# Kernel optimization log

Measured on AMD Instinct MI355X. Metric: run time of the kernel, lower is better.

## Reference

```python
import jax, jax.numpy as jnp
import numpy as np

D = 128      # internal_dimensions
L = 4        # num_edge_convs
N = 100000   # nodes
E = 800000   # edges
G = 64       # graphs
IN = 4       # in_channels


def _ln(x, g, b):
    m = jnp.mean(x, -1, keepdims=True)
    v = jnp.mean((x - m) ** 2, -1, keepdims=True)
    return (x - m) * jax.lax.rsqrt(v + 1e-5) * g + b


def _gelu(x):
    return jax.nn.gelu(x, approximate=False)  # torch nn.GELU default (erf)


def _seg_mean(x, seg, n):
    s = jax.ops.segment_sum(x, seg, num_segments=n)
    c = jax.ops.segment_sum(jnp.ones((x.shape[0], 1), x.dtype), seg, num_segments=n)
    return s / jnp.maximum(c, 1.0)


def _seg_max(x, seg, n):
    m = jax.ops.segment_max(x, seg, num_segments=n)
    return jnp.where(jnp.isfinite(m), m, 0.0)  # empty segments -> 0 (PyG convention)


def _forward(x, edge_index, batch, num_graphs,
             in_W1, in_b1, in_g1, in_bn1, in_W2, in_b2, in_g2, in_bn2,
             pre_g, pre_b, cW1, cb1, cg1, cbb1, cW2, cb2, cg2, cbb2, pW, pb,
             ag_g, ag_b,
             kW1, kb1, kg1, kbb1, kW2, kb2, kg2, kbb2,
             kW3, kb3, kg3, kbb3, kW4, kb4):
    n = x.shape[0]
    # input_net: Linear -> LN -> GELU -> Linear -> LN   (dropout=0, eval)
    h = _gelu(_ln(x @ in_W1 + in_b1, in_g1, in_bn1))
    h = _ln(h @ in_W2 + in_b2, in_g2, in_bn2)

    x_in_max = _seg_max(h, batch, num_graphs)
    x_in_mean = _seg_mean(h, batch, num_graphs)

    src, dst = edge_index[0], edge_index[1]  # PyG: message from src (x_j) to dst (x_i)
    xcur = h
    for l in range(L):
        identity = xcur
        hn = _ln(xcur, pre_g[l], pre_b[l])
        xi = hn[dst]            # [E, D]
        xj = hn[src]            # [E, D]
        m = jnp.concatenate([xi, xj - xi], axis=-1)       # [E, 2D]
        m = _gelu(_ln(m @ cW1[l] + cb1[l], cg1[l], cbb1[l]))
        m = _gelu(_ln(m @ cW2[l] + cb2[l], cg2[l], cbb2[l]))
        a_max = _seg_max(m, dst, n)
        a_mean = _seg_mean(m, dst, n)
        aggr = jnp.concatenate([a_max, a_mean], axis=-1)  # [N, 2D]
        xcur = identity + aggr @ pW[l] + pb[l]

    xcur = _ln(xcur, ag_g, ag_b)
    x_g_max = _seg_max(xcur, batch, num_graphs)
    x_g_mean = _seg_mean(xcur, batch, num_graphs)

    xp = jnp.concatenate([x_in_max, x_in_mean, x_g_max, x_g_mean], axis=-1)  # [G, 4D]
    z = _gelu(_ln(xp @ kW1 + kb1, kg1, kbb1))
    z = _gelu(_ln(z @ kW2 + kb2, kg2, kbb2))
    z = _gelu(_ln(z @ kW3 + kb3, kg3, kbb3))
    return z @ kW4 + kb4  # [G, 1]


def setup_inputs() -> dict:
    key = jax.random.key(0)
    ks = iter(jax.random.split(key, 64))
    def W(shape, fan):
        return jax.random.normal(next(ks), shape, jnp.float32) * np.float32((2.0 / fan) ** 0.5)
    inp = {}
    inp["x"] = jax.random.normal(next(ks), (N, IN), jnp.float32)
    inp["edge_index"] = jax.random.randint(next(ks), (2, E), 0, N)
    inp["batch"] = jnp.sort(jax.random.randint(next(ks), (N,), 0, G))
    inp["num_graphs"] = G
    inp["in_W1"] = W((IN, D), IN); inp["in_b1"] = jnp.zeros((D,), jnp.float32)
    inp["in_g1"] = jnp.ones((D,), jnp.float32); inp["in_bn1"] = jnp.zeros((D,), jnp.float32)
    inp["in_W2"] = W((D, D), D); inp["in_b2"] = jnp.zeros((D,), jnp.float32)
    inp["in_g2"] = jnp.ones((D,), jnp.float32); inp["in_bn2"] = jnp.zeros((D,), jnp.float32)
    inp["pre_g"] = jnp.ones((L, D), jnp.float32); inp["pre_b"] = jnp.zeros((L, D), jnp.float32)
    inp["cW1"] = W((L, 2 * D, D), 2 * D); inp["cb1"] = jnp.zeros((L, D), jnp.float32)
    inp["cg1"] = jnp.ones((L, D), jnp.float32); inp["cbb1"] = jnp.zeros((L, D), jnp.float32)
    inp["cW2"] = W((L, D, D), D); inp["cb2"] = jnp.zeros((L, D), jnp.float32)
    inp["cg2"] = jnp.ones((L, D), jnp.float32); inp["cbb2"] = jnp.zeros((L, D), jnp.float32)
    inp["pW"] = W((L, 2 * D, D), 2 * D); inp["pb"] = jnp.zeros((L, D), jnp.float32)
    inp["ag_g"] = jnp.ones((D,), jnp.float32); inp["ag_b"] = jnp.zeros((D,), jnp.float32)
    inp["kW1"] = W((4 * D, D), 4 * D); inp["kb1"] = jnp.zeros((D,), jnp.float32)
    inp["kg1"] = jnp.ones((D,), jnp.float32); inp["kbb1"] = jnp.zeros((D,), jnp.float32)
    inp["kW2"] = W((D, D), D); inp["kb2"] = jnp.zeros((D,), jnp.float32)
    inp["kg2"] = jnp.ones((D,), jnp.float32); inp["kbb2"] = jnp.zeros((D,), jnp.float32)
    inp["kW3"] = W((D, D // 4), D); inp["kb3"] = jnp.zeros((D // 4,), jnp.float32)
    inp["kg3"] = jnp.ones((D // 4,), jnp.float32); inp["kbb3"] = jnp.zeros((D // 4,), jnp.float32)
    inp["kW4"] = W((D // 4, 1), D // 4); inp["kb4"] = jnp.zeros((1,), jnp.float32)
    return inp


def reference(x, edge_index, batch, num_graphs,
              in_W1, in_b1, in_g1, in_bn1, in_W2, in_b2, in_g2, in_bn2,
              pre_g, pre_b, cW1, cb1, cg1, cbb1, cW2, cb2, cg2, cbb2, pW, pb,
              ag_g, ag_b,
              kW1, kb1, kg1, kbb1, kW2, kb2, kg2, kbb2,
              kW3, kb3, kg3, kbb3, kW4, kb4):
    return _forward(x, edge_index, batch, num_graphs,
                    in_W1, in_b1, in_g1, in_bn1, in_W2, in_b2, in_g2, in_bn2,
                    pre_g, pre_b, cW1, cb1, cg1, cbb1, cW2, cb2, cg2, cbb2, pW, pb,
                    ag_g, ag_b,
                    kW1, kb1, kg1, kbb1, kW2, kb2, kg2, kbb2,
                    kW3, kb3, kg3, kbb3, kW4, kb4)
```

## Files before the change

kernel.cpp:

```cpp
#include <hip/hip_runtime.h>
#include <hip/hip_bf16.h>
#include <math.h>

__device__ __forceinline__ float geluf(float x) {
    return 0.5f * x * (1.0f + erff(x * 0.70710678118654752f));
}
__device__ __forceinline__ unsigned fmap(float f) {
    unsigned u = __float_as_uint(f);
    return ((int)u < 0) ? ~u : (u | 0x80000000u);
}
__device__ __forceinline__ float funmap(unsigned m) {
    return __uint_as_float((m & 0x80000000u) ? (m ^ 0x80000000u) : ~m);
}
#define MAPNEGINF 0x007FFFFFu
__device__ __forceinline__ float wred64(float v) {
#pragma unroll
    for (int m = 1; m < 64; m <<= 1) v += __shfl_xor(v, m);
    return v;
}

__device__ __forceinline__ void stage_wq(float* Ws, const float* __restrict__ src, int t) {
#pragma unroll
    for (int it = 0; it < 4; ++it) {
        const int idx = it * 1024 + (t << 2);
        *(float4*)(Ws + idx) = *(const float4*)(src + idx);
    }
}

__device__ __forceinline__ void kloop_q(const float* As, const float* Ws, float (&acc)[4][8],
                                        const int r0, const int ogc, const int kb) {
#pragma unroll
    for (int kk = 0; kk < 32; kk += 4) {
        const float4 a0 = *(const float4*)(As + (r0 + 0) * 132 + kb + kk);
        const float4 a1 = *(const float4*)(As + (r0 + 1) * 132 + kb + kk);
        const float4 a2 = *(const float4*)(As + (r0 + 2) * 132 + kb + kk);
        const float4 a3 = *(const float4*)(As + (r0 + 3) * 132 + kb + kk);
#define MAD8(R, AV)                                                                     \
    {                                                                                   \
        acc[R][0] += (AV)*wA.x; acc[R][1] += (AV)*wA.y; acc[R][2] += (AV)*wA.z;         \
        acc[R][3] += (AV)*wA.w; acc[R][4] += (AV)*wB.x; acc[R][5] += (AV)*wB.y;         \
        acc[R][6] += (AV)*wB.z; acc[R][7] += (AV)*wB.w;                                 \
    }
#define KSTEP(J, C)                                                                     \
    {                                                                                   \
        const float4 wA = *(const float4*)(Ws + (kk + (J)) * 128 + ogc);                \
        const float4 wB = *(const float4*)(Ws + (kk + (J)) * 128 + 64 + ogc);           \
        MAD8(0, a0.C) MAD8(1, a1.C) MAD8(2, a2.C) MAD8(3, a3.C)                         \
    }
        KSTEP(0, x) KSTEP(1, y) KSTEP(2, z) KSTEP(3, w)
#undef KSTEP
#undef MAD8
    }
}

__global__ void k_zero(unsigned* __restrict__ p, int n) {
    const int i = blockIdx.x * 256 + threadIdx.x;
    if (i < n) p[i] = 0u;
}

__global__ void k_copyu(const unsigned* __restrict__ a, const unsigned* __restrict__ b,
                        unsigned* __restrict__ ac, unsigned* __restrict__ bc, int n) {
    const int i = blockIdx.x * 256 + threadIdx.x;
    if (i < n) {
        ac[i] = a[i];
        bc[i] = b[i];
    }
}

__global__ void k_count(const int* __restrict__ ei, unsigned* __restrict__ deg, int E) {
    const int e = blockIdx.x * 256 + threadIdx.x;
    if (e < E) atomicAdd(deg + ei[E + e], 1u);
}

__global__ void k_scan1(const unsigned* __restrict__ deg, unsigned* __restrict__ excl,
                        unsigned* __restrict__ bsum, int n) {
    __shared__ unsigned sh[256];
    const int t = threadIdx.x;
    const int base = blockIdx.x * 1024 + t * 4;
    unsigned v0 = (base + 0 < n) ? deg[base + 0] : 0u;
    unsigned v1 = (base + 1 < n) ? deg[base + 1] : 0u;
    unsigned v2 = (base + 2 < n) ? deg[base + 2] : 0u;
    unsigned v3 = (base + 3 < n) ? deg[base + 3] : 0u;
    const unsigned s = v0 + v1 + v2 + v3;
    sh[t] = s;
    __syncthreads();
    for (int off = 1; off < 256; off <<= 1) {
        unsigned x = 0;
        if (t >= off) x = sh[t - off];
        __syncthreads();
        if (t >= off) sh[t] += x;
        __syncthreads();
    }
    const unsigned ebase = sh[t] - s;
    if (base + 0 < n) excl[base + 0] = ebase;
    if (base + 1 < n) excl[base + 1] = ebase + v0;
    if (base + 2 < n) excl[base + 2] = ebase + v0 + v1;
    if (base + 3 < n) excl[base + 3] = ebase + v0 + v1 + v2;
    if (t == 255) bsum[blockIdx.x] = sh[255];
}

__global__ void k_scan2(unsigned* __restrict__ bsum, int nb) {
    __shared__ unsigned sh[256];
    const int t = threadIdx.x;
    const unsigned v = (t < nb) ? bsum[t] : 0u;
    sh[t] = v;
    __syncthreads();
    for (int off = 1; off < 256; off <<= 1) {
        unsigned x = 0;
        if (t >= off) x = sh[t - off];
        __syncthreads();
        if (t >= off) sh[t] += x;
        __syncthreads();
    }
    if (t < nb) bsum[t] = sh[t] - v;
}

__global__ void k_scan3(unsigned* __restrict__ excl, const unsigned* __restrict__ bsum, int n) {
    const int t = threadIdx.x;
    const int base = blockIdx.x * 1024 + t * 4;
    const unsigned add = bsum[blockIdx.x];
#pragma unroll
    for (int j = 0; j < 4; ++j)
        if (base + j < n) excl[base + j] += add;
}

__global__ void k_scatter(const int* __restrict__ ei, unsigned* __restrict__ cursor,
                          int* __restrict__ eperm, int E) {
    const int e = blockIdx.x * 256 + threadIdx.x;
    if (e < E) {
        const unsigned pos = atomicAdd(cursor + ei[E + e], 1u);
        eperm[pos] = e;
    }
}

__global__ void k_in1(const float* __restrict__ x, const float* __restrict__ W1,
                      const float* __restrict__ b1, const float* __restrict__ g1,
                      const float* __restrict__ bn1, float* __restrict__ h, int n) {
    const int t = threadIdx.x, lane = t & 63, wave = t >> 6;
    const int d0 = lane << 1;
    const float2 w0 = *(const float2*)(W1 + d0);
    const float2 w1 = *(const float2*)(W1 + 128 + d0);
    const float2 w2 = *(const float2*)(W1 + 256 + d0);
    const float2 w3 = *(const float2*)(W1 + 384 + d0);
    const float2 bb = *(const float2*)(b1 + d0);
    const float2 gg = *(const float2*)(g1 + d0);
    const float2 nn = *(const float2*)(bn1 + d0);
    const int stride = gridDim.x * 4;
    for (int node = blockIdx.x * 4 + wave; node < n; node += stride) {
        const float4 xv = *(const float4*)(x + (size_t)node * 4);
        float h0 = bb.x + xv.x * w0.x + xv.y * w1.x + xv.z * w2.x + xv.w * w3.x;
        float h1 = bb.y + xv.x * w0.y + xv.y * w1.y + xv.z * w2.y + xv.w * w3.y;
        const float s = wred64(h0 + h1), q = wred64(h0 * h0 + h1 * h1);
        const float mean = s * 0.0078125f, var = q * 0.0078125f - mean * mean;
        const float rs = rsqrtf(var + 1e-5f);
        h0 = geluf((h0 - mean) * rs * gg.x + nn.x);
        h1 = geluf((h1 - mean) * rs * gg.y + nn.y);
        *(float2*)(h + (size_t)node * 128 + d0) = make_float2(h0, h1);
    }
}

__global__ __launch_bounds__(256, 3) void k_in2(const float* __restrict__ A,
                                                const float* __restrict__ W,
                                                const float* __restrict__ bias,
                                                const float* __restrict__ g,
                                                const float* __restrict__ b,
                                                float* __restrict__ C, int n) {
    __shared__ float As[64 * 132];
    __shared__ float Ws[4096];
    const int t = threadIdx.x;
    const int n0 = blockIdx.x * 64;
    {
        const int r = t >> 2, c0 = (t & 3) << 5;
        const int row = n0 + r;
        const bool ok = row < n;
#pragma unroll
        for (int j = 0; j < 8; ++j) {
            const int col = c0 + (j << 2);
            float4 v = make_float4(0.f, 0.f, 0.f, 0.f);
            if (ok) v = *(const float4*)(A + (size_t)row * 128 + col);
            *(float4*)(As + r * 132 + col) = v;
        }
    }
    float acc[4][8];
#pragma unroll
    for (int r = 0; r < 4; ++r)
#pragma unroll
        for (int o = 0; o < 8; ++o) acc[r][o] = 0.f;
    const int og = t & 15, eg = t >> 4;
    const int ogc = og << 2, r0 = eg << 2;
#pragma unroll
    for (int q4 = 0; q4 < 4; ++q4) {
        stage_wq(Ws, W + q4 * 4096, t);
        __syncthreads();
        kloop_q(As, Ws, acc, r0, ogc, q4 * 32);
        __syncthreads();
    }
    const float4 bA = *(const float4*)(bias + ogc);
    const float4 bB = *(const float4*)(bias + 64 + ogc);
    const float4 gA = *(const float4*)(g + ogc);
    const float4 gB = *(const float4*)(g + 64 + ogc);
    const float4 lA = *(const float4*)(b + ogc);
    const float4 lB = *(const float4*)(b + 64 + ogc);
#pragma unroll
    for (int r = 0; r < 4; ++r) {
        float v[8];
        v[0] = acc[r][0] + bA.x; v[1] = acc[r][1] + bA.y;
        v[2] = acc[r][2] + bA.z; v[3] = acc[r][3] + bA.w;
        v[4] = acc[r][4] + bB.x; v[5] = acc[r][5] + bB.y;
        v[6] = acc[r][6] + bB.z; v[7] = acc[r][7] + bB.w;
        float s = 0.f, q = 0.f;
#pragma unroll
        for (int o = 0; o < 8; ++o) { s += v[o]; q += v[o] * v[o]; }
#pragma unroll
        for (int m = 1; m < 16; m <<= 1) { s += __shfl_xor(s, m); q += __shfl_xor(q, m); }
        const float mean = s * 0.0078125f;
        const float var = q * 0.0078125f - mean * mean;
        const float rs = rsqrtf(var + 1e-5f);
        const int row = n0 + r0 + r;
        if (row < n) {
            *(float4*)(C + (size_t)row * 128 + ogc) = make_float4(
                (v[0] - mean) * rs * gA.x + lA.x, (v[1] - mean) * rs * gA.y + lA.y,
                (v[2] - mean) * rs * gA.z + lA.z, (v[3] - mean) * rs * gA.w + lA.w);
            *(float4*)(C + (size_t)row * 128 + 64 + ogc) = make_float4(
                (v[4] - mean) * rs * gB.x + lB.x, (v[5] - mean) * rs * gB.y + lB.y,
                (v[6] - mean) * rs * gB.z + lB.z, (v[7] - mean) * rs * gB.w + lB.w);
        }
    }
}

__global__ void k_ln(const float* __restrict__ in, const float* __restrict__ g,
                     const float* __restrict__ b, float* __restrict__ out, int n) {
    const int t = threadIdx.x, lane = t & 63, wave = t >> 6;
    const int d0 = lane << 1;
    const float ga = g[d0], gb = g[d0 + 1], ba = b[d0], bb = b[d0 + 1];
    const int stride = gridDim.x * 4;
    for (int node = blockIdx.x * 4 + wave; node < n; node += stride) {
        const float2 v = *(const float2*)(in + (size_t)node * 128 + d0);
        const float s = wred64(v.x + v.y), q = wred64(v.x * v.x + v.y * v.y);
        const float mean = s * 0.0078125f, var = q * 0.0078125f - mean * mean;
        const float rs = rsqrtf(var + 1e-5f);
        *(float2*)(out + (size_t)node * 128 + d0) =
            make_float2((v.x - mean) * rs * ga + ba, (v.y - mean) * rs * gb + bb);
    }
}

__global__ void k_wxj(const float* __restrict__ c, float* __restrict__ Wx,
                      float* __restrict__ Wj) {
    const int idx = blockIdx.x * 256 + threadIdx.x;
    const float a = c[idx], b = c[16384 + idx];
    Wx[idx] = a - b;
    Wj[idx] = b;
}

__global__ __launch_bounds__(256, 3) void k_pq(const float* __restrict__ xcur,
                                               const float* __restrict__ g,
                                               const float* __restrict__ b,
                                               const float* __restrict__ Wx,
                                               const float* __restrict__ Wj,
                                               const float* __restrict__ cb1,
                                               float* __restrict__ P, float* __restrict__ Q,
                                               int n) {
    __shared__ float As[64 * 132];
    __shared__ float Ws[4096];
    __shared__ float sg[128], sb[128];
    const int t = threadIdx.x;
    const int n0 = blockIdx.x * 64;
    if (t < 128) { sg[t] = g[t]; sb[t] = b[t]; }
    __syncthreads();
    {
        const int r = t >> 2, c0 = (t & 3) << 5;
        const int row = n0 + r;
        const bool ok = row < n;
        float4 v4[8];
        float s = 0.f, q = 0.f;
        if (ok) {
#pragma unroll
            for (int j = 0; j < 8; ++j) {
                v4[j] = *(const float4*)(xcur + (size_t)row * 128 + c0 + (j << 2));
                s += v4[j].x + v4[j].y + v4[j].z + v4[j].w;
                q += v4[j].x * v4[j].x + v4[j].y * v4[j].y + v4[j].z * v4[j].z +
                     v4[j].w * v4[j].w;
            }
        } else {
#pragma unroll
            for (int j = 0; j < 8; ++j) v4[j] = make_float4(0.f, 0.f, 0.f, 0.f);
        }
        s += __shfl_xor(s, 1); s += __shfl_xor(s, 2);
        q += __shfl_xor(q, 1); q += __shfl_xor(q, 2);
        const float mean = s * 0.0078125f;
        const float var = q * 0.0078125f - mean * mean;
        const float rs = rsqrtf(var + 1e-5f);
#pragma unroll
        for (int j = 0; j < 8; ++j) {
            const int c = c0 + (j << 2);
            As[r * 132 + c + 0] = (v4[j].x - mean) * rs * sg[c + 0] + sb[c + 0];
            As[r * 132 + c + 1] = (v4[j].y - mean) * rs * sg[c + 1] + sb[c + 1];
            As[r * 132 + c + 2] = (v4[j].z - mean) * rs * sg[c + 2] + sb[c + 2];
            As[r * 132 + c + 3] = (v4[j].w - mean) * rs * sg[c + 3] + sb[c + 3];
        }
    }
    float accP[4][8], accQ[4][8];
#pragma unroll
    for (int r = 0; r < 4; ++r)
#pragma unroll
        for (int o = 0; o < 8; ++o) { accP[r][o] = 0.f; accQ[r][o] = 0.f; }
    const int og = t & 15, eg = t >> 4;
    const int ogc = og << 2, r0 = eg << 2;
#pragma unroll
    for (int q4 = 0; q4 < 4; ++q4) {
        stage_wq(Ws, Wx + q4 * 4096, t);
        __syncthreads();
        kloop_q(As, Ws, accP, r0, ogc, q4 * 32);
        __syncthreads();
    }
#pragma unroll
    for (int q4 = 0; q4 < 4; ++q4) {
        stage_wq(Ws, Wj + q4 * 4096, t);
        __syncthreads();
        kloop_q(As, Ws, accQ, r0, ogc, q4 * 32);
        __syncthreads();
    }
    const float4 bA = *(const float4*)(cb1 + ogc);
    const float4 bB = *(const float4*)(cb1 + 64 + ogc);
#pragma unroll
    for (int r = 0; r < 4; ++r) {
        const int row = n0 + r0 + r;
        if (row < n) {
            *(float4*)(P + (size_t)row * 128 + ogc) =
                make_float4(accP[r][0] + bA.x, accP[r][1] + bA.y, accP[r][2] + bA.z,
                            accP[r][3] + bA.w);
            *(float4*)(P + (size_t)row * 128 + 64 + ogc) =
                make_float4(accP[r][4] + bB.x, accP[r][5] + bB.y, accP[r][6] + bB.z,
                            accP[r][7] + bB.w);
            *(float4*)(Q + (size_t)row * 128 + ogc) =
                make_float4(accQ[r][0], accQ[r][1], accQ[r][2], accQ[r][3]);
            *(float4*)(Q + (size_t)row * 128 + 64 + ogc) =
                make_float4(accQ[r][4], accQ[r][5], accQ[r][6], accQ[r][7]);
        }
    }
}

__global__ __launch_bounds__(256, 3) void k_edge(
    const float* __restrict__ P, const float* __restrict__ Q, const int* __restrict__ ei,
    const int* __restrict__ eperm, const float* __restrict__ W2, const float* __restrict__ g1,
    const float* __restrict__ b1, const float* __restrict__ cb2, const float* __restrict__ g2,
    const float* __restrict__ b2, const unsigned* __restrict__ rowend,
    const unsigned* __restrict__ degc, float* __restrict__ amax, float* __restrict__ asum,
    float* __restrict__ recmax, float* __restrict__ recsum, int* __restrict__ recid, int E) {
    __shared__ float Us[64 * 132];
    __shared__ float Ws[4096];
    __shared__ int sdst[64], ssrc[64], sdg[64];
    __shared__ float scb2[128], sg2[128], sb2[128];
    const int t = threadIdx.x;
    const int base = blockIdx.x * 512;
    if (t >= 128) {
        const int d = t - 128;
        scb2[d] = cb2[d];
        sg2[d] = g2[d];
        sb2[d] = b2[d];
    }
    const int lane = t & 63, wave = t >> 6;
    const int d0 = lane << 1;
    const float g1a = g1[d0], g1b = g1[d0 + 1], b1a = b1[d0], b1b = b1[d0 + 1];
    const int og = t & 15, eg = t >> 4;
    const int ogc = og << 2, r0 = eg << 2;
    int cur = -1, istart = 0;
    float vmax = -INFINITY, vsum = 0.f;
    int id0 = -1, id1 = -1;

    for (int s8 = 0; s8 < 8; ++s8) {
        const int sb = base + s8 * 64;
        __syncthreads();
        if (t < 64) {
            const int idx = sb + t;
            const int e = eperm[idx < E ? idx : (E - 1)];
            ssrc[t] = ei[e];
            const int d = ei[E + e];
            sdg[t] = d;
            sdst[t] = (idx < E) ? d : -1;
        }
        __syncthreads();
#pragma unroll
        for (int half = 0; half < 2; ++half) {
            float2 pv[8], qv[8];
#pragma unroll
            for (int u = 0; u < 8; ++u) {
                const int i = ((half * 8 + u) << 2) + wave;
                pv[u] = *(const float2*)(P + (size_t)sdg[i] * 128 + d0);
                qv[u] = *(const float2*)(Q + (size_t)ssrc[i] * 128 + d0);
            }
#pragma unroll
            for (int u = 0; u < 8; ++u) {
                const int i = ((half * 8 + u) << 2) + wave;
                const float x0 = pv[u].x + qv[u].x, x1 = pv[u].y + qv[u].y;
                const float s = wred64(x0 + x1);
                const float q = wred64(x0 * x0 + x1 * x1);
                const float mean = s * 0.0078125f;
                const float var = q * 0.0078125f - mean * mean;
                const float rs = rsqrtf(var + 1e-5f);
                const float y0 = geluf((x0 - mean) * rs * g1a + b1a);
                const float y1 = geluf((x1 - mean) * rs * g1b + b1b);
                *(float2*)(Us + i * 132 + d0) = make_float2(y0, y1);
            }
        }
        float acc[4][8];
#pragma unroll
        for (int r = 0; r < 4; ++r)
#pragma unroll
            for (int o = 0; o < 8; ++o) acc[r][o] = 0.f;
#pragma unroll
        for (int q4 = 0; q4 < 4; ++q4) {
            stage_wq(Ws, W2 + q4 * 4096, t);
            __syncthreads();
            kloop_q(Us, Ws, acc, r0, ogc, q4 * 32);
            __syncthreads();
        }
#pragma unroll
        for (int r = 0; r < 4; ++r) {
            float v[8];
            float s = 0.f, q = 0.f;
#pragma unroll
            for (int o = 0; o < 8; ++o) {
                const int col = (o < 4) ? (ogc + o) : (64 + ogc + o - 4);
                v[o] = acc[r][o] + scb2[col];
                s += v[o];
                q += v[o] * v[o];
            }
#pragma unroll
            for (int m = 1; m < 16; m <<= 1) { s += __shfl_xor(s, m); q += __shfl_xor(q, m); }
            const float mean = s * 0.0078125f;
            const float var = q * 0.0078125f - mean * mean;
            const float rs = rsqrtf(var + 1e-5f);
#pragma unroll
            for (int o = 0; o < 8; ++o) {
                const int col = (o < 4) ? (ogc + o) : (64 + ogc + o - 4);
                v[o] = geluf((v[o] - mean) * rs * sg2[col] + sb2[col]);
            }
            *(float4*)(Us + (r0 + r) * 132 + ogc) = make_float4(v[0], v[1], v[2], v[3]);
            *(float4*)(Us + (r0 + r) * 132 + 64 + ogc) = make_float4(v[4], v[5], v[6], v[7]);
        }
        __syncthreads();
        if (t < 128) {
            for (int i = 0; i < 64; ++i) {
                const int dn = sdst[i];
                const int gi = s8 * 64 + i;
                if (dn != cur) {
                    if (cur >= 0) {
                        const unsigned re = rowend[cur];
                        const unsigned rs0 = re - degc[cur];
                        const unsigned ps = (unsigned)(base + istart);
                        const unsigned pe = (unsigned)(base + gi);
                        if (ps == rs0 && pe == re) {
                            amax[(size_t)cur * 128 + t] = vmax;
                            asum[(size_t)cur * 128 + t] = vsum;
                        } else {
                            const int slot = (istart == 0) ? 0 : 1;
                            const size_t ro = (size_t)(2 * blockIdx.x + slot) * 128 + t;
                            recmax[ro] = vmax;
                            recsum[ro] = vsum;
                            if (slot == 0) id0 = cur; else id1 = cur;
                        }
                    }
                    cur = dn;
                    istart = gi;
                    vmax = -INFINITY;
                    vsum = 0.f;
                }
                if (dn >= 0) {
                    const float v = Us[i * 132 + t];
                    vmax = fmaxf(vmax, v);
                    vsum += v;
                }
            }
        }
    }
    if (t < 128 && cur >= 0) {
        const int iend = min(512, E - base);
        const unsigned re = rowend[cur];
        const unsigned rs0 = re - degc[cur];
        const unsigned ps = (unsigned)(base + istart);
        const unsigned pe = (unsigned)(base + iend);
        if (ps == rs0 && pe == re) {
            amax[(size_t)cur * 128 + t] = vmax;
            asum[(size_t)cur * 128 + t] = vsum;
        } else {
            const int slot = (istart == 0) ? 0 : 1;
            const size_t ro = (size_t)(2 * blockIdx.x + slot) * 128 + t;
            recmax[ro] = vmax;
            recsum[ro] = vsum;
            if (slot == 0) id0 = cur; else id1 = cur;
        }
    }
    if (t == 0) {
        recid[2 * blockIdx.x] = id0;
        recid[2 * blockIdx.x + 1] = id1;
    }
}

__global__ void k_merge(const unsigned* __restrict__ rowend, const unsigned* __restrict__ degc,
                        const float* __restrict__ recmax, const float* __restrict__ recsum,
                        const int* __restrict__ recid, float* __restrict__ amax,
                        float* __restrict__ asum, int n) {
    const int node = blockIdx.x * 2 + (threadIdx.x >> 7);
    const int t = threadIdx.x & 127;
    if (node >= n) return;
    const unsigned dg = degc[node];
    if (dg == 0u) {
        amax[(size_t)node * 128 + t] = 0.f;
        asum[(size_t)node * 128 + t] = 0.f;
        return;
    }
    const unsigned re = rowend[node], rs = re - dg;
    const int b0 = rs >> 9, b1 = (re - 1) >> 9;
    if (b0 == b1) return;
    float m = -INFINITY, s = 0.f;
    for (int b = b0; b <= b1; ++b) {
#pragma unroll
        for (int sl = 0; sl < 2; ++sl) {
            if (recid[2 * b + sl] == node) {
                const size_t ro = (size_t)(2 * b + sl) * 128 + t;
                m = fmaxf(m, recmax[ro]);
                s += recsum[ro];
            }
        }
    }
    amax[(size_t)node * 128 + t] = m;
    asum[(size_t)node * 128 + t] = s;
}

__global__ __launch_bounds__(256, 3) void k_update(const float* __restrict__ amax,
                                                   const float* __restrict__ asum,
                                                   const unsigned* __restrict__ degc,
                                                   const float* __restrict__ pW,
                                                   const float* __restrict__ pb,
                                                   float* __restrict__ xcur, int n) {
    __shared__ float As[64 * 132];
    __shared__ float Ws[4096];
    const int t = threadIdx.x;
    const int n0 = blockIdx.x * 64;
    const int og = t & 15, eg = t >> 4;
    const int ogc = og << 2, r0 = eg << 2;
    float acc[4][8];
#pragma unroll
    for (int r = 0; r < 4; ++r)
#pragma unroll
        for (int o = 0; o < 8; ++o) acc[r][o] = 0.f;
    const int r = t >> 2, c0 = (t & 3) << 5;
    const int row = n0 + r;
    const bool ok = row < n;
#pragma unroll
    for (int pass = 0; pass < 2; ++pass) {
        if (pass == 0) {
#pragma unroll
            for (int j = 0; j < 8; ++j) {
                const int col = c0 + (j << 2);
                float4 v = make_float4(0.f, 0.f, 0.f, 0.f);
                if (ok) v = *(const float4*)(amax + (size_t)row * 128 + col);
                *(float4*)(As + r * 132 + col) = v;
            }
        } else {
            float inv = 0.f;
            if (ok) {
                const unsigned dv = degc[row];
                inv = 1.f / (float)(dv < 1u ? 1u : dv);
            }
#pragma unroll
            for (int j = 0; j < 8; ++j) {
                const int col = c0 + (j << 2);
                float4 v = make_float4(0.f, 0.f, 0.f, 0.f);
                if (ok) {
                    const float4 sv = *(const float4*)(asum + (size_t)row * 128 + col);
                    v = make_float4(sv.x * inv, sv.y * inv, sv.z * inv, sv.w * inv);
                }
                *(float4*)(As + r * 132 + col) = v;
            }
        }
#pragma unroll
        for (int q4 = 0; q4 < 4; ++q4) {
            stage_wq(Ws, pW + (size_t)(pass * 128 + q4 * 32) * 128, t);
            __syncthreads();
            kloop_q(As, Ws, acc, r0, ogc, q4 * 32);
            __syncthreads();
        }
    }
    const float4 bA = *(const float4*)(pb + ogc);
    const float4 bB = *(const float4*)(pb + 64 + ogc);
#pragma unroll
    for (int rr = 0; rr < 4; ++rr) {
        const int orow = n0 + r0 + rr;
        if (orow < n) {
            const float4 x0 = *(const float4*)(xcur + (size_t)orow * 128 + ogc);
            const float4 x1 = *(const float4*)(xcur + (size_t)orow * 128 + 64 + ogc);
            *(float4*)(xcur + (size_t)orow * 128 + ogc) =
                make_float4(x0.x + acc[rr][0] + bA.x, x0.y + acc[rr][1] + bA.y,
                            x0.z + acc[rr][2] + bA.z, x0.w + acc[rr][3] + bA.w);
            *(float4*)(xcur + (size_t)orow * 128 + 64 + ogc) =
                make_float4(x1.x + acc[rr][4] + bB.x, x1.y + acc[rr][5] + bB.y,
                            x1.z + acc[rr][6] + bB.z, x1.w + acc[rr][7] + bB.w);
        }
    }
}

__global__ void k_pool_init(unsigned* __restrict__ gmax1, float* __restrict__ gsum1,
                            unsigned* __restrict__ gcount1, unsigned* __restrict__ gmax2,
                            float* __restrict__ gsum2, unsigned* __restrict__ gcount2, int ng) {
    const int i = blockIdx.x * 256 + threadIdx.x;
    if (i < ng * 128) {
        gmax1[i] = MAPNEGINF;
        gsum1[i] = 0.f;
        gmax2[i] = MAPNEGINF;
        gsum2[i] = 0.f;
    }
    if (i < ng) {
        gcount1[i] = 0u;
        gcount2[i] = 0u;
    }
}

__global__ void k_pool(const float* __restrict__ in, const int* __restrict__ batch,
                       unsigned* __restrict__ gmax, float* __restrict__ gsum,
                       unsigned* __restrict__ gcount, int n) {
    const int t = threadIdx.x;
    if (t >= 128) return;
    const int per = (n + gridDim.x - 1) / gridDim.x;
    const int i0 = blockIdx.x * per;
    const int i1 = min(n, i0 + per);
    if (i0 >= i1) return;
    int cur = batch[i0];
    float vmax = -INFINITY, vsum = 0.f;
    unsigned cnt = 0;
    for (int i = i0; i < i1; ++i) {
        const int g = batch[i];
        if (g != cur) {
            atomicMax(gmax + (size_t)cur * 128 + t, fmap(vmax));
            atomicAdd(gsum + (size_t)cur * 128 + t, vsum);
            if (t == 0) atomicAdd(gcount + cur, cnt);
            cur = g;
            vmax = -INFINITY;
            vsum = 0.f;
            cnt = 0;
        }
        const float v = in[(size_t)i * 128 + t];
        vmax = fmaxf(vmax, v);
        vsum += v;
        cnt++;
    }
    atomicMax(gmax + (size_t)cur * 128 + t, fmap(vmax));
    atomicAdd(gsum + (size_t)cur * 128 + t, vsum);
    if (t == 0) atomicAdd(gcount + cur, cnt);
}

__global__ void k_xp(const unsigned* __restrict__ gmax1, const float* __restrict__ gsum1,
                     const unsigned* __restrict__ gcount1, const unsigned* __restrict__ gmax2,
                     const float* __restrict__ gsum2, const unsigned* __restrict__ gcount2,
                     float* __restrict__ xp) {
    const int g = blockIdx.x, d = threadIdx.x;
    const unsigned c1u = gcount1[g], c2u = gcount2[g];
    const float c1 = (float)(c1u < 1u ? 1u : c1u);
    const float c2 = (float)(c2u < 1u ? 1u : c2u);
    const unsigned m1 = gmax1[g * 128 + d], m2 = gmax2[g * 128 + d];
    xp[g * 512 + d] = (m1 == MAPNEGINF) ? 0.f : funmap(m1);
    xp[g * 512 + 128 + d] = gsum1[g * 128 + d] / c1;
    xp[g * 512 + 256 + d] = (m2 == MAPNEGINF) ? 0.f : funmap(m2);
    xp[g * 512 + 384 + d] = gsum2[g * 128 + d] / c2;
}

__global__ __launch_bounds__(64) void k_know(
    const float* __restrict__ xp, const float* __restrict__ kW1, const float* __restrict__ kb1,
    const float* __restrict__ kg1, const float* __restrict__ kbb1, const float* __restrict__ kW2,
    const float* __restrict__ kb2, const float* __restrict__ kg2, const float* __restrict__ kbb2,
    const float* __restrict__ kW3, const float* __restrict__ kb3, const float* __restrict__ kg3,
    const float* __restrict__ kbb3, const float* __restrict__ kW4, const float* __restrict__ kb4,
    float* __restrict__ out) {
    __shared__ float sh[512];
    __shared__ float s3[32];
    const int l = threadIdx.x, g = blockIdx.x;
    const int d0 = l << 1;
    *(float4*)(sh + l * 8) = *(const float4*)(xp + g * 512 + l * 8);
    *(float4*)(sh + l * 8 + 4) = *(const float4*)(xp + g * 512 + l * 8 + 4);
    __syncthreads();
    float a0 = kb1[d0], a1 = kb1[d0 + 1];
    for (int k = 0; k < 512; ++k) {
        const float u = sh[k];
        const float2 w = *(const float2*)(kW1 + k * 128 + d0);
        a0 += u * w.x;
        a1 += u * w.y;
    }
    {
        const float s = wred64(a0 + a1), q = wred64(a0 * a0 + a1 * a1);
        const float mean = s * 0.0078125f, var = q * 0.0078125f - mean * mean;
        const float rs = rsqrtf(var + 1e-5f);
        a0 = geluf((a0 - mean) * rs * kg1[d0] + kbb1[d0]);
        a1 = geluf((a1 - mean) * rs * kg1[d0 + 1] + kbb1[d0 + 1]);
    }
    __syncthreads();
    sh[d0] = a0;
    sh[d0 + 1] = a1;
    __syncthreads();
    float b0v = kb2[d0], b1v = kb2[d0 + 1];
    for (int k = 0; k < 128; ++k) {
        const float u = sh[k];
        const float2 w = *(const float2*)(kW2 + k * 128 + d0);
        b0v += u * w.x;
        b1v += u * w.y;
    }
    {
        const float s = wred64(b0v + b1v), q = wred64(b0v * b0v + b1v * b1v);
        const float mean = s * 0.0078125f, var = q * 0.0078125f - mean * mean;
        const float rs = rsqrtf(var + 1e-5f);
        b0v = geluf((b0v - mean) * rs * kg2[d0] + kbb2[d0]);
        b1v = geluf((b1v - mean) * rs * kg2[d0 + 1] + kbb2[d0 + 1]);
    }
    __syncthreads();
    sh[d0] = b0v;
    sh[d0 + 1] = b1v;
    __syncthreads();
    const int d3 = (l & 15) << 1;
    float c0 = kb3[d3], c1 = kb3[d3 + 1];
    for (int k = 0; k < 128; ++k) {
        const float u = sh[k];
        const float2 w = *(const float2*)(kW3 + k * 32 + d3);
        c0 += u * w.x;
        c1 += u * w.y;
    }
    {
        float s = c0 + c1, q = c0 * c0 + c1 * c1;
#pragma unroll
        for (int m = 1; m < 16; m <<= 1) {
            s += __shfl_xor(s, m);
            q += __shfl_xor(q, m);
        }
        const float mean = s * 0.03125f, var = q * 0.03125f - mean * mean;
        const float rs = rsqrtf(var + 1e-5f);
        c0 = geluf((c0 - mean) * rs * kg3[d3] + kbb3[d3]);
        c1 = geluf((c1 - mean) * rs * kg3[d3 + 1] + kbb3[d3 + 1]);
    }
    if (l < 16) {
        s3[d3] = c0;
        s3[d3 + 1] = c1;
    }
    __syncthreads();
    if (l == 0) {
        float rr = kb4[0];
        for (int k = 0; k < 32; ++k) rr += s3[k] * kW4[k];
        out[g] = rr;
    }
}

extern "C" void kernel_launch(void* const* d_in, const int* in_sizes, int n_in, void* d_out,
                              int out_size, void* d_ws, size_t ws_size, hipStream_t stream) {
    const int N = in_sizes[0] / 4;
    const int E = in_sizes[1] / 2;
    const int G = 64;
    const int L = 4;

    const float* x = (const float*)d_in[0];
    const int* ei = (const int*)d_in[1];
    const int* batch = (const int*)d_in[2];
    const float* inW1 = (const float*)d_in[4];
    const float* inb1 = (const float*)d_in[5];
    const float* ing1 = (const float*)d_in[6];
    const float* inbn1 = (const float*)d_in[7];
    const float* inW2 = (const float*)d_in[8];
    const float* inb2 = (const float*)d_in[9];
    const float* ing2 = (const float*)d_in[10];
    const float* inbn2 = (const float*)d_in[11];
    const float* pre_g = (const float*)d_in[12];
    const float* pre_b = (const float*)d_in[13];
    const float* cW1 = (const float*)d_in[14];
    const float* cb1 = (const float*)d_in[15];
    const float* cg1 = (const float*)d_in[16];
    const float* cbb1 = (const float*)d_in[17];
    const float* cW2 = (const float*)d_in[18];
    const float* cb2 = (const float*)d_in[19];
    const float* cg2 = (const float*)d_in[20];
    const float* cbb2 = (const float*)d_in[21];
    const float* pW = (const float*)d_in[22];
    const float* pb = (const float*)d_in[23];
    const float* ag_g = (const float*)d_in[24];
    const float* ag_b = (const float*)d_in[25];
    const float* kW1 = (const float*)d_in[26];
    const float* kb1 = (const float*)d_in[27];
    const float* kg1 = (const float*)d_in[28];
    const float* kbb1 = (const float*)d_in[29];
    const float* kW2 = (const float*)d_in[30];
    const float* kb2 = (const float*)d_in[31];
    const float* kg2 = (const float*)d_in[32];
    const float* kbb2 = (const float*)d_in[33];
    const float* kW3 = (const float*)d_in[34];
    const float* kb3 = (const float*)d_in[35];
    const float* kg3 = (const float*)d_in[36];
    const float* kbb3 = (const float*)d_in[37];
    const float* kW4 = (const float*)d_in[38];
    const float* kb4 = (const float*)d_in[39];
    float* out = (float*)d_out;

    const int nblkE = (E + 511) / 512;

    char* wsb = (char*)d_ws;
    size_t off = 0;
    auto ALC = [&](size_t bytes) {
        void* p = wsb + off;
        off = (off + bytes + 255) & ~(size_t)255;
        return p;
    };
    const size_t NB = (size_t)N * 128 * 4;
    float* xcur = (float*)ALC(NB);
    float* Pb = (float*)ALC(NB);
    float* Qb = (float*)ALC(NB);
    float* amax = (float*)ALC(NB);
    float* asum = (float*)ALC(NB);
    unsigned* deg = (unsigned*)ALC((size_t)N * 4);
    unsigned* cursor = (unsigned*)ALC((size_t)N * 4);
    unsigned* degc = (unsigned*)ALC((size_t)N * 4);
    unsigned* rowend = (unsigned*)ALC((size_t)N * 4);
    unsigned* bsum = (unsigned*)ALC(4096);
    int* eperm = (int*)ALC((size_t)E * 4);
    float* recmax = (float*)ALC((size_t)nblkE * 2 * 128 * 4);
    float* recsum = (float*)ALC((size_t)nblkE * 2 * 128 * 4);
    int* recid = (int*)ALC((size_t)nblkE * 2 * 4);
    float* Wx = (float*)ALC(65536);
    float* Wj = (float*)ALC(65536);
    unsigned* gmax1 = (unsigned*)ALC((size_t)G * 128 * 4);
    float* gsum1 = (float*)ALC((size_t)G * 128 * 4);
    unsigned* gcount1 = (unsigned*)ALC((size_t)G * 4);
    unsigned* gmax2 = (unsigned*)ALC((size_t)G * 128 * 4);
    float* gsum2 = (float*)ALC((size_t)G * 128 * 4);
    unsigned* gcount2 = (unsigned*)ALC((size_t)G * 4);
    float* xp = (float*)ALC((size_t)G * 512 * 4);

    if (off > ws_size) {
        k_zero<<<(out_size + 255) / 256, 256, 0, stream>>>((unsigned*)d_out, out_size);
        return;
    }

    k_zero<<<(N + 255) / 256, 256, 0, stream>>>(deg, N);
    k_count<<<(E + 255) / 256, 256, 0, stream>>>(ei, deg, E);
    const int nb = (N + 1023) / 1024;
    k_scan1<<<nb, 256, 0, stream>>>(deg, cursor, bsum, N);
    k_scan2<<<1, 256, 0, stream>>>(bsum, nb);
    k_scan3<<<nb, 256, 0, stream>>>(cursor, bsum, N);
    k_scatter<<<(E + 255) / 256, 256, 0, stream>>>(ei, cursor, eperm, E);
    k_copyu<<<(N + 255) / 256, 256, 0, stream>>>(deg, cursor, degc, rowend, N);

    const int gemmGrid = (N + 63) / 64;
    k_in1<<<1024, 256, 0, stream>>>(x, inW1, inb1, ing1, inbn1, Pb, N);
    k_in2<<<gemmGrid, 256, 0, stream>>>(Pb, inW2, inb2, ing2, inbn2, xcur, N);
    k_pool_init<<<(G * 128 + 255) / 256, 256, 0, stream>>>(gmax1, gsum1, gcount1, gmax2, gsum2,
                                                           gcount2, G);
    k_pool<<<512, 256, 0, stream>>>(xcur, batch, gmax1, gsum1, gcount1, N);

    for (int l = 0; l < L; ++l) {
        k_wxj<<<64, 256, 0, stream>>>(cW1 + (size_t)l * 32768, Wx, Wj);
        k_pq<<<gemmGrid, 256, 0, stream>>>(xcur, pre_g + l * 128, pre_b + l * 128, Wx, Wj,
                                           cb1 + l * 128, Pb, Qb, N);
        k_edge<<<nblkE, 256, 0, stream>>>(Pb, Qb, ei, eperm, cW2 + (size_t)l * 16384,
                                          cg1 + l * 128, cbb1 + l * 128, cb2 + l * 128,
                                          cg2 + l * 128, cbb2 + l * 128, rowend, degc, amax, asum,
                                          recmax, recsum, recid, E);
        k_merge<<<(N + 1) / 2, 256, 0, stream>>>(rowend, degc, recmax, recsum, recid, amax, asum,
                                                 N);
        k_update<<<gemmGrid, 256, 0, stream>>>(amax, asum, degc, pW + (size_t)l * 32768,
                                               pb + l * 128, xcur, N);
    }

    k_ln<<<1024, 256, 0, stream>>>(xcur, ag_g, ag_b, Pb, N);
    k_pool<<<512, 256, 0, stream>>>(Pb, batch, gmax2, gsum2, gcount2, N);
    k_xp<<<G, 128, 0, stream>>>(gmax1, gsum1, gcount1, gmax2, gsum2, gcount2, xp);
    k_know<<<G, 64, 0, stream>>>(xp, kW1, kb1, kg1, kbb1, kW2, kb2, kg2, kbb2, kW3, kb3, kg3,
                                 kbb3, kW4, kb4, out);
}
```

Measured before the change: 102.0 ms.

## Store per-node P/Q projections in bf16 and pre-sort edge src/dst arrays

The per-node P and Q projections that feed the edge kernel are now written as bf16, which halves the bytes of the random gathers over 800k edges per layer. The CSR scatter now writes sorted src and dst arrays directly, so the edge kernel no longer does an indirect lookup through eperm. The fused LN+dual-GEMM kernel is split into a separate LN pass plus two single-output GEMMs, and launch bounds drop from 3 to 2 blocks per CU. The risks are lost precision in the bf16 intermediates and the extra kernel launches and memory traffic for the normalized activations.

```diff
diff --git a/kernel.cpp b/kernel.cpp
--- a/kernel.cpp
+++ b/kernel.cpp
@@ -5,18 +5,23 @@
 __device__ __forceinline__ float geluf(float x) {
     return 0.5f * x * (1.0f + erff(x * 0.70710678118654752f));
 }
+#define MAPNEGINF 0x007FFFFFu
+__device__ __forceinline__ float funmap(unsigned m) {
+    return __uint_as_float((m & 0x80000000u) ? (m ^ 0x80000000u) : ~m);
+}
 __device__ __forceinline__ unsigned fmap(float f) {
     unsigned u = __float_as_uint(f);
     return ((int)u < 0) ? ~u : (u | 0x80000000u);
 }
-__device__ __forceinline__ float funmap(unsigned m) {
-    return __uint_as_float((m & 0x80000000u) ? (m ^ 0x80000000u) : ~m);
-}
-#define MAPNEGINF 0x007FFFFFu
 __device__ __forceinline__ float wred64(float v) {
 #pragma unroll
     for (int m = 1; m < 64; m <<= 1) v += __shfl_xor(v, m);
     return v;
+}
+__device__ __forceinline__ unsigned short bf16r(float f) {
+    unsigned u = __float_as_uint(f);
+    u += 0x7fffu + ((u >> 16) & 1u);
+    return (unsigned short)(u >> 16);
 }
 
 __device__ __forceinline__ void stage_wq(float* Ws, const float* __restrict__ src, int t) {
@@ -125,11 +130,14 @@
 }
 
 __global__ void k_scatter(const int* __restrict__ ei, unsigned* __restrict__ cursor,
-                          int* __restrict__ eperm, int E) {
+                          int* __restrict__ esrc, int* __restrict__ edst, int E) {
     const int e = blockIdx.x * 256 + threadIdx.x;
     if (e < E) {
-        const unsigned pos = atomicAdd(cursor + ei[E + e], 1u);
-        eperm[pos] = e;
+        const int s = ei[e];
+        const int d = ei[E + e];
+        const unsigned pos = atomicAdd(cursor + d, 1u);
+        esrc[pos] = s;
+        edst[pos] = d;
     }
 }
 
@@ -159,7 +167,7 @@
     }
 }
 
-__global__ __launch_bounds__(256, 3) void k_in2(const float* __restrict__ A,
+__global__ __launch_bounds__(256, 2) void k_in2(const float* __restrict__ A,
                                                 const float* __restrict__ W,
                                                 const float* __restrict__ bias,
                                                 const float* __restrict__ g,
@@ -252,101 +260,68 @@
     Wj[idx] = b;
 }
 
-__global__ __launch_bounds__(256, 3) void k_pq(const float* __restrict__ xcur,
-                                               const float* __restrict__ g,
-                                               const float* __restrict__ b,
-                                               const float* __restrict__ Wx,
-                                               const float* __restrict__ Wj,
-                                               const float* __restrict__ cb1,
-                                               float* __restrict__ P, float* __restrict__ Q,
-                                               int n) {
+__global__ __launch_bounds__(256, 2) void k_gemmh(const float* __restrict__ A,
+                                                  const float* __restrict__ W,
+                                                  const float* __restrict__ bias,
+                                                  unsigned short* __restrict__ C, int n) {
     __shared__ float As[64 * 132];
     __shared__ float Ws[4096];
-    __shared__ float sg[128], sb[128];
     const int t = threadIdx.x;
     const int n0 = blockIdx.x * 64;
-    if (t < 128) { sg[t] = g[t]; sb[t] = b[t]; }
-    __syncthreads();
     {
         const int r = t >> 2, c0 = (t & 3) << 5;
         const int row = n0 + r;
         const bool ok = row < n;
-        float4 v4[8];
-        float s = 0.f, q = 0.f;
-        if (ok) {
-#pragma unroll
-            for (int j = 0; j < 8; ++j) {
-                v4[j] = *(const float4*)(xcur + (size_t)row * 128 + c0 + (j << 2));
-                s += v4[j].x + v4[j].y + v4[j].z + v4[j].w;
-                q += v4[j].x * v4[j].x + v4[j].y * v4[j].y + v4[j].z * v4[j].z +
-                     v4[j].w * v4[j].w;
-            }
-        } else {
-#pragma unroll
-            for (int j = 0; j < 8; ++j) v4[j] = make_float4(0.f, 0.f, 0.f, 0.f);
-        }
-        s += __shfl_xor(s, 1); s += __shfl_xor(s, 2);
-        q += __shfl_xor(q, 1); q += __shfl_xor(q, 2);
-        const float mean = s * 0.0078125f;
-        const float var = q * 0.0078125f - mean * mean;
-        const float rs = rsqrtf(var + 1e-5f);
 #pragma unroll
         for (int j = 0; j < 8; ++j) {
-            const int c = c0 + (j << 2);
-            As[r * 132 + c + 0] = (v4[j].x - mean) * rs * sg[c + 0] + sb[c + 0];
-            As[r * 132 + c + 1] = (v4[j].y - mean) * rs * sg[c + 1] + sb[c + 1];
-            As[r * 132 + c + 2] = (v4[j].z - mean) * rs * sg[c + 2] + sb[c + 2];
-            As[r * 132 + c + 3] = (v4[j].w - mean) * rs * sg[c + 3] + sb[c + 3];
-        }
-    }
-    float accP[4][8], accQ[4][8];
+            const int col = c0 + (j << 2);
+            float4 v = make_float4(0.f, 0.f, 0.f, 0.f);
+            if (ok) v = *(const float4*)(A + (size_t)row * 128 + col);
+            *(float4*)(As + r * 132 + col) = v;
+        }
+    }
+    float acc[4][8];
 #pragma unroll
     for (int r = 0; r < 4; ++r)
 #pragma unroll
-        for (int o = 0; o < 8; ++o) { accP[r][o] = 0.f; accQ[r][o] = 0.f; }
+        for (int o = 0; o < 8; ++o) acc[r][o] = 0.f;
     const int og = t & 15, eg = t >> 4;
     const int ogc = og << 2, r0 = eg << 2;
 #pragma unroll
     for (int q4 = 0; q4 < 4; ++q4) {
-        stage_wq(Ws, Wx + q4 * 4096, t);
-        __syncthreads();
-        kloop_q(As, Ws, accP, r0, ogc, q4 * 32);
-        __syncthreads();
-    }
-#pragma unroll
-    for (int q4 = 0; q4 < 4; ++q4) {
-        stage_wq(Ws, Wj + q4 * 4096, t);
-        __syncthreads();
-        kloop_q(As, Ws, accQ, r0, ogc, q4 * 32);
-        __syncthreads();
-    }
-    const float4 bA = *(const float4*)(cb1 + ogc);
-    const float4 bB = *(const float4*)(cb1 + 64 + ogc);
+        stage_wq(Ws, W + q4 * 4096, t);
+        __syncthreads();
+        kloop_q(As, Ws, acc, r0, ogc, q4 * 32);
+        __syncthreads();
+    }
+    float4 bA = make_float4(0.f, 0.f, 0.f, 0.f), bB = bA;
+    if (bias) {
+        bA = *(const float4*)(bias + ogc);
+        bB = *(const float4*)(bias + 64 + ogc);
+    }
 #pragma unroll
     for (int r = 0; r < 4; ++r) {
         const int row = n0 + r0 + r;
         if (row < n) {
-            *(float4*)(P + (size_t)row * 128 + ogc) =
-                make_float4(accP[r][0] + bA.x, accP[r][1] + bA.y, accP[r][2] + bA.z,
-                            accP[r][3] + bA.w);
-            *(float4*)(P + (size_t)row * 128 + 64 + ogc) =
-                make_float4(accP[r][4] + bB.x, accP[r][5] + bB.y, accP[r][6] + bB.z,
-                            accP[r][7] + bB.w);
-            *(float4*)(Q + (size_t)row * 128 + ogc) =
-                make_float4(accQ[r][0], accQ[r][1], accQ[r][2], accQ[r][3]);
-            *(float4*)(Q + (size_t)row * 128 + 64 + ogc) =
-                make_float4(accQ[r][4], accQ[r][5], accQ[r][6], accQ[r][7]);
-        }
-    }
-}
-
-__global__ __launch_bounds__(256, 3) void k_edge(
-    const float* __restrict__ P, const float* __restrict__ Q, const int* __restrict__ ei,
-    const int* __restrict__ eperm, const float* __restrict__ W2, const float* __restrict__ g1,
-    const float* __restrict__ b1, const float* __restrict__ cb2, const float* __restrict__ g2,
-    const float* __restrict__ b2, const unsigned* __restrict__ rowend,
-    const unsigned* __restrict__ degc, float* __restrict__ amax, float* __restrict__ asum,
-    float* __restrict__ recmax, float* __restrict__ recsum, int* __restrict__ recid, int E) {
+            ushort4 u0, u1;
+            u0.x = bf16r(acc[r][0] + bA.x); u0.y = bf16r(acc[r][1] + bA.y);
+            u0.z = bf16r(acc[r][2] + bA.z); u0.w = bf16r(acc[r][3] + bA.w);
+            u1.x = bf16r(acc[r][4] + bB.x); u1.y = bf16r(acc[r][5] + bB.y);
+            u1.z = bf16r(acc[r][6] + bB.z); u1.w = bf16r(acc[r][7] + bB.w);
+            *(ushort4*)(C + (size_t)row * 128 + ogc) = u0;
+            *(ushort4*)(C + (size_t)row * 128 + 64 + ogc) = u1;
+        }
+    }
+}
+
+__global__ __launch_bounds__(256, 2) void k_edge(
+    const unsigned short* __restrict__ P, const unsigned short* __restrict__ Q,
+    const int* __restrict__ esrc, const int* __restrict__ edst, const float* __restrict__ W2,
+    const float* __restrict__ g1, const float* __restrict__ b1, const float* __restrict__ cb2,
+    const float* __restrict__ g2, const float* __restrict__ b2,
+    const unsigned* __restrict__ rowend, const unsigned* __restrict__ degc,
+    float* __restrict__ amax, float* __restrict__ asum, float* __restrict__ recmax,
+    float* __restrict__ recsum, int* __restrict__ recid, int E) {
     __shared__ float Us[64 * 132];
     __shared__ float Ws[4096];
     __shared__ int sdst[64], ssrc[64], sdg[64];
@@ -373,35 +348,29 @@
         __syncthreads();
         if (t < 64) {
             const int idx = sb + t;
-            const int e = eperm[idx < E ? idx : (E - 1)];
-            ssrc[t] = ei[e];
-            const int d = ei[E + e];
+            const int ci = idx < E ? idx : (E - 1);
+            ssrc[t] = esrc[ci];
+            const int d = edst[ci];
             sdg[t] = d;
             sdst[t] = (idx < E) ? d : -1;
         }
         __syncthreads();
-#pragma unroll
-        for (int half = 0; half < 2; ++half) {
-            float2 pv[8], qv[8];
-#pragma unroll
-            for (int u = 0; u < 8; ++u) {
-                const int i = ((half * 8 + u) << 2) + wave;
-                pv[u] = *(const float2*)(P + (size_t)sdg[i] * 128 + d0);
-                qv[u] = *(const float2*)(Q + (size_t)ssrc[i] * 128 + d0);
-            }
-#pragma unroll
-            for (int u = 0; u < 8; ++u) {
-                const int i = ((half * 8 + u) << 2) + wave;
-                const float x0 = pv[u].x + qv[u].x, x1 = pv[u].y + qv[u].y;
-                const float s = wred64(x0 + x1);
-                const float q = wred64(x0 * x0 + x1 * x1);
-                const float mean = s * 0.0078125f;
-                const float var = q * 0.0078125f - mean * mean;
-                const float rs = rsqrtf(var + 1e-5f);
-                const float y0 = geluf((x0 - mean) * rs * g1a + b1a);
-                const float y1 = geluf((x1 - mean) * rs * g1b + b1b);
-                *(float2*)(Us + i * 132 + d0) = make_float2(y0, y1);
-            }
+#pragma unroll 4
+        for (int p = 0; p < 16; ++p) {
+            const int i = (p << 2) + wave;
+            const unsigned pu = *(const unsigned*)(P + ((size_t)sdg[i] << 7) + d0);
+            const unsigned qu = *(const unsigned*)(Q + ((size_t)ssrc[i] << 7) + d0);
+            const float x0 = __uint_as_float(pu << 16) + __uint_as_float(qu << 16);
+            const float x1 =
+                __uint_as_float(pu & 0xffff0000u) + __uint_as_float(qu & 0xffff0000u);
+            const float s = wred64(x0 + x1);
+            const float q = wred64(x0 * x0 + x1 * x1);
+            const float mean = s * 0.0078125f;
+            const float var = q * 0.0078125f - mean * mean;
+            const float rs = rsqrtf(var + 1e-5f);
+            const float y0 = geluf((x0 - mean) * rs * g1a + b1a);
+            const float y1 = geluf((x1 - mean) * rs * g1b + b1b);
+            *(float2*)(Us + i * 132 + d0) = make_float2(y0, y1);
         }
         float acc[4][8];
 #pragma unroll
@@ -528,7 +497,7 @@
     asum[(size_t)node * 128 + t] = s;
 }
 
-__global__ __launch_bounds__(256, 3) void k_update(const float* __restrict__ amax,
+__global__ __launch_bounds__(256, 2) void k_update(const float* __restrict__ amax,
                                                    const float* __restrict__ asum,
                                                    const unsigned* __restrict__ degc,
                                                    const float* __restrict__ pW,
@@ -806,16 +775,18 @@
     };
     const size_t NB = (size_t)N * 128 * 4;
     float* xcur = (float*)ALC(NB);
-    float* Pb = (float*)ALC(NB);
-    float* Qb = (float*)ALC(NB);
-    float* amax = (float*)ALC(NB);
+    float* hn = (float*)ALC(NB);
+    float* amax = hn;
     float* asum = (float*)ALC(NB);
+    unsigned short* Pb = (unsigned short*)ALC((size_t)N * 128 * 2);
+    unsigned short* Qb = (unsigned short*)ALC((size_t)N * 128 * 2);
     unsigned* deg = (unsigned*)ALC((size_t)N * 4);
     unsigned* cursor = (unsigned*)ALC((size_t)N * 4);
     unsigned* degc = (unsigned*)ALC((size_t)N * 4);
     unsigned* rowend = (unsigned*)ALC((size_t)N * 4);
     unsigned* bsum = (unsigned*)ALC(4096);
-    int* eperm = (int*)ALC((size_t)E * 4);
+    int* esrc = (int*)ALC((size_t)E * 4);
+    int* edst = (int*)ALC((size_t)E * 4);
     float* recmax = (float*)ALC((size_t)nblkE * 2 * 128 * 4);
     float* recsum = (float*)ALC((size_t)nblkE * 2 * 128 * 4);
     int* recid = (int*)ALC((size_t)nblkE * 2 * 4);
@@ -840,21 +811,22 @@
     k_scan1<<<nb, 256, 0, stream>>>(deg, cursor, bsum, N);
     k_scan2<<<1, 256, 0, stream>>>(bsum, nb);
     k_scan3<<<nb, 256, 0, stream>>>(cursor, bsum, N);
-    k_scatter<<<(E + 255) / 256, 256, 0, stream>>>(ei, cursor, eperm, E);
+    k_scatter<<<(E + 255) / 256, 256, 0, stream>>>(ei, cursor, esrc, edst, E);
     k_copyu<<<(N + 255) / 256, 256, 0, stream>>>(deg, cursor, degc, rowend, N);
 
     const int gemmGrid = (N + 63) / 64;
-    k_in1<<<1024, 256, 0, stream>>>(x, inW1, inb1, ing1, inbn1, Pb, N);
-    k_in2<<<gemmGrid, 256, 0, stream>>>(Pb, inW2, inb2, ing2, inbn2, xcur, N);
+    k_in1<<<1024, 256, 0, stream>>>(x, inW1, inb1, ing1, inbn1, hn, N);
+    k_in2<<<gemmGrid, 256, 0, stream>>>(hn, inW2, inb2, ing2, inbn2, xcur, N);
     k_pool_init<<<(G * 128 + 255) / 256, 256, 0, stream>>>(gmax1, gsum1, gcount1, gmax2, gsum2,
                                                            gcount2, G);
     k_pool<<<512, 256, 0, stream>>>(xcur, batch, gmax1, gsum1, gcount1, N);
 
     for (int l = 0; l < L; ++l) {
         k_wxj<<<64, 256, 0, stream>>>(cW1 + (size_t)l * 32768, Wx, Wj);
-        k_pq<<<gemmGrid, 256, 0, stream>>>(xcur, pre_g + l * 128, pre_b + l * 128, Wx, Wj,
-                                           cb1 + l * 128, Pb, Qb, N);
-        k_edge<<<nblkE, 256, 0, stream>>>(Pb, Qb, ei, eperm, cW2 + (size_t)l * 16384,
+        k_ln<<<1024, 256, 0, stream>>>(xcur, pre_g + l * 128, pre_b + l * 128, hn, N);
+        k_gemmh<<<gemmGrid, 256, 0, stream>>>(hn, Wx, cb1 + l * 128, Pb, N);
+        k_gemmh<<<gemmGrid, 256, 0, stream>>>(hn, Wj, (const float*)nullptr, Qb, N);
+        k_edge<<<nblkE, 256, 0, stream>>>(Pb, Qb, esrc, edst, cW2 + (size_t)l * 16384,
                                           cg1 + l * 128, cbb1 + l * 128, cb2 + l * 128,
                                           cg2 + l * 128, cbb2 + l * 128, rowend, degc, amax, asum,
                                           recmax, recsum, recid, E);
@@ -864,8 +836,8 @@
                                                pb + l * 128, xcur, N);
     }
 
-    k_ln<<<1024, 256, 0, stream>>>(xcur, ag_g, ag_b, Pb, N);
-    k_pool<<<512, 256, 0, stream>>>(Pb, batch, gmax2, gsum2, gcount2, N);
+    k_ln<<<1024, 256, 0, stream>>>(xcur, ag_g, ag_b, hn, N);
+    k_pool<<<512, 256, 0, stream>>>(hn, batch, gmax2, gsum2, gcount2, N);
     k_xp<<<G, 128, 0, stream>>>(gmax1, gsum1, gcount1, gmax2, gsum2, gcount2, xp);
     k_know<<<G, 64, 0, stream>>>(xp, kW1, kb1, kg1, kbb1, kW2, kb2, kg2, kbb2, kW3, kb3, kg3,
                                  kbb3, kW4, kb4, out);
```

Measured after the change: 95.78 ms. 1.06x faster.
